# Optimization experiments

Measured on AMD Instinct MI355X. Metric: run time of the kernel, lower is better.

Reference implementation:

```python
import jax, jax.numpy as jnp
import numpy as np

EPS = 1e-5
DIM_HEAD = 64
HEADS = 8

def layernorm(x, gamma, beta):
    mu = jnp.mean(x, axis=-1, keepdims=True)
    var = jnp.var(x, axis=-1, keepdims=True)
    return (x - mu) * jax.lax.rsqrt(var + EPS) * gamma + beta

def setup_inputs() -> dict:
    key = jax.random.key(0)
    ks = jax.random.split(key, 8)
    b, n, dh = 1, 896, 3072       # batch, enformer seq len, enformer_hidden_dim
    c, j, dc = 64, 127, 1024      # num contexts (tracks), context len, context_dim
    inner = HEADS * DIM_HEAD      # 512
    return {
        "embeddings": jax.random.normal(ks[0], (b, n, dh), jnp.float32),
        "context": jax.random.normal(ks[1], (c, j, dc), jnp.float32),
        "context_mask": jax.random.randint(ks[2], (b, j), 0, 2) > 0,
        "q_gamma": jnp.ones((dh,), jnp.float32),
        "q_beta": jnp.zeros((dh,), jnp.float32),
        "kv_gamma": jnp.ones((dc,), jnp.float32),
        "kv_beta": jnp.zeros((dc,), jnp.float32),
        "Wq": jax.random.normal(ks[3], (dh, inner), jnp.float32) * 0.02,
        "Wkv": jax.random.normal(ks[4], (dc, 2 * inner), jnp.float32) * 0.02,
        "null_k": jax.random.normal(ks[5], (inner,), jnp.float32),
        "null_v": jax.random.normal(ks[6], (inner,), jnp.float32),
        "Wo": jax.random.normal(ks[7], (inner, dh), jnp.float32) * 0.02,
        "bo": jnp.zeros((dh,), jnp.float32),
        "Wp": jax.random.normal(jax.random.fold_in(key, 9), (dh, 1), jnp.float32) * 0.02,
        "bp": jnp.zeros((1,), jnp.float32),
    }

def reference(embeddings, context, context_mask, q_gamma, q_beta, kv_gamma, kv_beta,
              Wq, Wkv, null_k, null_v, Wo, bo, Wp, bp):
    h, d = HEADS, DIM_HEAD
    scale = d ** -0.5
    b, n, dh = embeddings.shape
    c = context.shape[0]
    # projections
    q = layernorm(embeddings, q_gamma, q_beta) @ Wq            # (b, n, h*d)
    kv = layernorm(context, kv_gamma, kv_beta) @ Wkv           # (c, j, 2*h*d)
    k, v = jnp.split(kv, 2, axis=-1)
    # prepend null key/value token
    k = jnp.concatenate([jnp.broadcast_to(null_k, (c, 1, h * d)), k], axis=1)
    v = jnp.concatenate([jnp.broadcast_to(null_v, (c, 1, h * d)), v], axis=1)
    # split heads: (b, h, i, d) / (c, h, j, d)
    q = q.reshape(b, n, h, d).transpose(0, 2, 1, 3)
    k = k.reshape(c, -1, h, d).transpose(0, 2, 1, 3)
    v = v.reshape(c, -1, h, d).transpose(0, 2, 1, 3)
    sim = jnp.einsum('bhid,chjd->bchij', q, k) * scale         # (b, c, h, i, j+1)
    # mask: pad with True for the null token, broadcast over c, h, i
    mask = jnp.pad(context_mask, ((0, 0), (1, 0)), constant_values=True)
    sim = jnp.where(mask[:, None, None, None, :], sim, -jnp.finfo(sim.dtype).max)
    attn = jax.nn.softmax(sim, axis=-1)
    out = jnp.einsum('bchij,chjd->bchid', attn, v)             # (b, c, h, i, d)
    out = out.transpose(0, 1, 3, 2, 4).reshape(b, c, n, h * d)  # (b, c, n, h*d)
    branch = out @ Wo + bo                                     # (b, c, n, dh)
    emb = embeddings[:, None] + branch                         # (b, c, n, dh)
    pred = jax.nn.softplus((emb @ Wp + bp)[..., 0])            # (b, c, n)
    return pred.transpose(0, 2, 1)                             # (b, n, c)
```

## Files before the change

### kernel.cpp

```cpp
#include <hip/hip_runtime.h>
#include <math.h>

#define N_SEQ   896
#define DH      3072
#define NCTX    64
#define JLEN    127
#define DC      1024
#define HEADS   8
#define DHEAD   64
#define INNER   512
#define MKV     8128
#define MKVPAD  8192

typedef __bf16 bf16x8 __attribute__((ext_vector_type(8)));
typedef float  f32x4  __attribute__((ext_vector_type(4)));

#define OFF_EDOT   0LL
#define OFF_QBF    (OFF_EDOT + N_SEQ)
#define OFF_KBF    (OFF_QBF  + (long long)N_SEQ*INNER/2)
#define OFF_VPM    (OFF_KBF  + (long long)NCTX*128*INNER/2)
#define OFF_VPNULL (OFF_VPM  + (long long)MKV*8)
#define OFF_WOP    (OFF_VPNULL + 8)
#define OFF_BOP    (OFF_WOP  + INNER)
#define OFF_SBUF   (OFF_BOP  + 16)
#define OFF_ANQ    (OFF_SBUF + (long long)NCTX*HEADS*N_SEQ)
#define OFF_ANKV   (OFF_ANQ  + (long long)N_SEQ*DH/2)
#define OFF_WQT    (OFF_ANKV + (long long)MKVPAD*DC/2)
#define OFF_WKT    (OFF_WQT  + (long long)INNER*DH/2)
#define OFF_WVPT   (OFF_WKT  + (long long)INNER*DC/2)
#define OFF_QSL    (OFF_WVPT + 16*1024/2)

__device__ __forceinline__ void async_copy16(const __bf16* g, __bf16* l) {
    __builtin_amdgcn_global_load_lds(
        (const __attribute__((address_space(1))) unsigned int*)g,
        (__attribute__((address_space(3))) unsigned int*)l,
        16, 0, 0);
}

template <int P>
__global__ __launch_bounds__(256)
void ln_bf16_kernel(const float* __restrict__ X,
                    const float* __restrict__ gamma, const float* __restrict__ beta,
                    const float* __restrict__ wp,
                    __bf16* __restrict__ out, float* __restrict__ dotout) {
    const int K = P * 1024;
    int row = blockIdx.x;
    const float* x = X + (long long)row * K;
    float4 xv[P];
    float s = 0.f, ss = 0.f, dp = 0.f;
    #pragma unroll
    for (int p = 0; p < P; ++p) {
        xv[p] = *(const float4*)&x[p * 1024 + threadIdx.x * 4];
        s  += xv[p].x + xv[p].y + xv[p].z + xv[p].w;
        ss += xv[p].x * xv[p].x + xv[p].y * xv[p].y
            + xv[p].z * xv[p].z + xv[p].w * xv[p].w;
        if (wp) {
            float4 w4 = *(const float4*)&wp[p * 1024 + threadIdx.x * 4];
            dp += xv[p].x * w4.x + xv[p].y * w4.y + xv[p].z * w4.z + xv[p].w * w4.w;
        }
    }
    #pragma unroll
    for (int o = 32; o > 0; o >>= 1) {
        s  += __shfl_down(s,  o);
        ss += __shfl_down(ss, o);
        dp += __shfl_down(dp, o);
    }
    __shared__ float red[3][4];
    __shared__ float sh_mu, sh_rstd;
    int lane = threadIdx.x & 63, w = threadIdx.x >> 6;
    if (lane == 0) { red[0][w] = s; red[1][w] = ss; red[2][w] = dp; }
    __syncthreads();
    if (threadIdx.x == 0) {
        float S  = red[0][0] + red[0][1] + red[0][2] + red[0][3];
        float SS = red[1][0] + red[1][1] + red[1][2] + red[1][3];
        float m = S / K;
        sh_mu = m;
        sh_rstd = rsqrtf(SS / K - m * m + 1e-5f);
        if (dotout) dotout[row] = red[2][0] + red[2][1] + red[2][2] + red[2][3];
    }
    __syncthreads();
    float m = sh_mu, r = sh_rstd;
    __bf16* o = out + (long long)row * K;
    #pragma unroll
    for (int p = 0; p < P; ++p) {
        int col = p * 1024 + threadIdx.x * 4;
        float4 g4 = *(const float4*)&gamma[col];
        float4 b4 = *(const float4*)&beta[col];
        __bf16 ov[4];
        ov[0] = (__bf16)((xv[p].x - m) * r * g4.x + b4.x);
        ov[1] = (__bf16)((xv[p].y - m) * r * g4.y + b4.y);
        ov[2] = (__bf16)((xv[p].z - m) * r * g4.z + b4.z);
        ov[3] = (__bf16)((xv[p].w - m) * r * g4.w + b4.w);
        *(ushort4*)&o[col] = *(ushort4*)ov;
    }
}

__global__ __launch_bounds__(256)
void transpose_bf16_kernel(const float* __restrict__ B, int R, int C,
                           __bf16* __restrict__ Bt) {
    __shared__ float t[32][33];
    int rb = blockIdx.x * 32, cb = blockIdx.y * 32;
    int tx = threadIdx.x & 31, ty = threadIdx.x >> 5;
    #pragma unroll
    for (int i = 0; i < 32; i += 8)
        t[ty + i][tx] = B[(long long)(rb + ty + i) * C + cb + tx];
    __syncthreads();
    #pragma unroll
    for (int i = 0; i < 32; i += 8)
        Bt[(long long)(cb + ty + i) * R + rb + tx] = (__bf16)t[tx][ty + i];
}

__global__ void wop_kernel(const float* __restrict__ Wo, const float* __restrict__ bo,
                           const float* __restrict__ Wp, float* __restrict__ wop,
                           float* __restrict__ bop) {
    int r = blockIdx.x;
    const float* src = (r < INNER) ? (Wo + (long long)r * DH) : bo;
    float s = 0.f;
    for (int k = threadIdx.x; k < DH; k += blockDim.x) s += src[k] * Wp[k];
    for (int o = 32; o > 0; o >>= 1) s += __shfl_down(s, o);
    __shared__ float red[4];
    int lane = threadIdx.x & 63, w = threadIdx.x >> 6;
    if (lane == 0) red[w] = s;
    __syncthreads();
    if (threadIdx.x == 0) {
        float S = red[0] + red[1] + red[2] + red[3];
        if (r < INNER) wop[r] = S; else *bop = S;
    }
}

__global__ void wvp_kernel(const float* __restrict__ Wkv, const float* __restrict__ wop,
                           const float* __restrict__ null_v, const float* __restrict__ null_k,
                           __bf16* __restrict__ wvpt, float* __restrict__ vpnull,
                           __bf16* __restrict__ k_bf) {
    int bx = blockIdx.x;
    if (bx < 32) {
        int t = bx * 256 + threadIdx.x;
        int k = t >> 3, h = t & 7;
        const float* src = Wkv + (long long)k * (2 * INNER) + INNER + h * 64;
        const float* wv  = wop + h * 64;
        float s = 0.f;
        #pragma unroll 16
        for (int d = 0; d < 64; ++d) s += src[d] * wv[d];
        wvpt[h * 1024 + k] = (__bf16)s;
    } else {
        for (int i = threadIdx.x; i < 8 * 1024; i += 256)
            wvpt[8 * 1024 + i] = (__bf16)0.f;
        for (int i = threadIdx.x; i < NCTX * INNER; i += 256) {
            int c = i >> 9, d = i & 511;
            k_bf[(long long)(c * 128) * INNER + d] = (__bf16)null_k[d];
        }
        if (threadIdx.x < 8) {
            int h = threadIdx.x;
            float s = 0.f;
            #pragma unroll 16
            for (int d = 0; d < 64; ++d) s += null_v[h * 64 + d] * wop[h * 64 + d];
            vpnull[h] = s;
        }
    }
}

__global__ __launch_bounds__(256)
void proj_kernel(const __bf16* __restrict__ ANQ, const __bf16* __restrict__ WQT,
                 const __bf16* __restrict__ ANKV, const __bf16* __restrict__ WKT,
                 const __bf16* __restrict__ WVPT,
                 float* __restrict__ qsl, __bf16* __restrict__ kout,
                 float* __restrict__ vpm) {
    __shared__ __align__(16) __bf16 As[128 * 32];
    __shared__ __align__(16) __bf16 Bs[128 * 32];
    int b = blockIdx.x;
    int tid = threadIdx.x;
    int lane = tid & 63, w = tid >> 6;
    int n16 = lane & 15, quad = lane >> 4;
    int wr = (w >> 1) * 64, wc = (w & 1) * 64;

    const __bf16 *A, *B;
    int K, kbeg, kend, mode, slice = 0;
    long long m0, n0;
    if (b < 224) {
        mode = 0; slice = b / 28;
        int rem = b % 28;
        m0 = (long long)(rem % 7) * 128;
        n0 = (long long)(rem / 7) * 128;
        K = DH; kbeg = slice * 384; kend = kbeg + 384;
        A = ANQ; B = WQT;
    } else {
        mode = 1;
        int b2 = b - 224;
        m0 = (long long)(b2 & 63) * 128;
        n0 = (long long)(b2 >> 6) * 128;
        K = DC; kbeg = 0; kend = DC;
        A = ANKV; B = WKT;
    }
    bool dovp = (mode == 1) && (n0 == 0);

    const __bf16* aG = A + (m0 + (tid >> 2)) * K + (tid & 3) * 8;
    const __bf16* bG = B + (n0 + (tid >> 2)) * K + (tid & 3) * 8;
    __bf16* aL = As + tid * 8;
    __bf16* bL = Bs + tid * 8;

    f32x4 acc[4][4], accv[4];
    const f32x4 z = {0.f, 0.f, 0.f, 0.f};
    #pragma unroll
    for (int i = 0; i < 4; ++i) {
        accv[i] = z;
        #pragma unroll
        for (int j = 0; j < 4; ++j) acc[i][j] = z;
    }

    for (int k0 = kbeg; k0 < kend; k0 += 32) {
        async_copy16(aG + k0, aL);
        async_copy16(aG + (long long)64 * K + k0, aL + 2048);
        async_copy16(bG + k0, bL);
        async_copy16(bG + (long long)64 * K + k0, bL + 2048);
        bf16x8 bv;
        if (dovp) bv = *(const bf16x8*)&WVPT[n16 * 1024 + k0 + quad * 8];
        __syncthreads();
        bf16x8 af[4], bfr[4];
        #pragma unroll
        for (int i = 0; i < 4; ++i)
            af[i]  = *(const bf16x8*)&As[(wr + i * 16 + n16) * 32 + quad * 8];
        #pragma unroll
        for (int j = 0; j < 4; ++j)
            bfr[j] = *(const bf16x8*)&Bs[(wc + j * 16 + n16) * 32 + quad * 8];
        #pragma unroll
        for (int i = 0; i < 4; ++i)
            #pragma unroll
            for (int j = 0; j < 4; ++j)
                acc[i][j] = __builtin_amdgcn_mfma_f32_16x16x32_bf16(af[i], bfr[j], acc[i][j], 0, 0, 0);
        if (dovp) {
            #pragma unroll
            for (int i = 0; i < 4; ++i)
                accv[i] = __builtin_amdgcn_mfma_f32_16x16x32_bf16(af[i], bv, accv[i], 0, 0, 0);
        }
        __syncthreads();
    }

    if (mode == 0) {
        float* qdst = qsl + (long long)slice * (N_SEQ * INNER);
        #pragma unroll
        for (int i = 0; i < 4; ++i)
            #pragma unroll
            for (int r = 0; r < 4; ++r) {
                long long gr = m0 + wr + i * 16 + quad * 4 + r;
                #pragma unroll
                for (int j = 0; j < 4; ++j) {
                    long long gc = n0 + wc + j * 16 + n16;
                    qdst[gr * INNER + gc] = acc[i][j][r];
                }
            }
    } else {
        #pragma unroll
        for (int i = 0; i < 4; ++i)
            #pragma unroll
            for (int r = 0; r < 4; ++r) {
                long long gr = m0 + wr + i * 16 + quad * 4 + r;
                if (gr >= MKV) continue;
                int cc = (int)(gr / JLEN), jj = (int)(gr % JLEN);
                #pragma unroll
                for (int j = 0; j < 4; ++j) {
                    long long gc = n0 + wc + j * 16 + n16;
                    kout[((long long)(cc * 128) + jj + 1) * INNER + gc] = (__bf16)acc[i][j][r];
                }
                if (dovp && n16 < 8) vpm[gr * 8 + n16] = accv[i][r];
            }
    }
}

__global__ void qreduce_kernel(const float* __restrict__ qsl, __bf16* __restrict__ qbf) {
    int t = blockIdx.x * 256 + threadIdx.x;
    float s = 0.f;
    #pragma unroll
    for (int k = 0; k < 8; ++k) s += qsl[(long long)k * (N_SEQ * INNER) + t];
    qbf[t] = (__bf16)s;
}

__global__ __launch_bounds__(256)
void attn_mfma_kernel(const __bf16* __restrict__ qb, const __bf16* __restrict__ kb,
                      const float* __restrict__ vpm, const float* __restrict__ vpnull,
                      const int* __restrict__ mask, float* __restrict__ s_buf) {
    int h = blockIdx.x & 7, c = blockIdx.x >> 3;
    int tid = threadIdx.x;
    int lane = tid & 63, w = tid >> 6;
    int n16 = lane & 15, quad = lane >> 4;

    const __bf16* kbase = kb + (long long)(c * 128) * INNER + h * DHEAD;
    bf16x8 bF[8][2];
    #pragma unroll
    for (int t = 0; t < 8; ++t)
        #pragma unroll
        for (int s = 0; s < 2; ++s)
            bF[t][s] = *(const bf16x8*)(kbase + (long long)(t * 16 + n16) * INNER + s * 32 + quad * 8);

    float vpv[8], am[8];
    #pragma unroll
    for (int t = 0; t < 8; ++t) {
        int col = t * 16 + n16;
        vpv[t] = (col == 0) ? vpnull[h] : vpm[(long long)(c * JLEN + col - 1) * 8 + h];
        am[t]  = (col == 0) ? 0.f : (mask[col - 1] ? 0.f : -3.0e38f);
    }

    const __bf16* qbase = qb + h * DHEAD;
    const f32x4 zero = {0.f, 0.f, 0.f, 0.f};
    for (int it = 0; it < 14; ++it) {
        int r0 = (it * 4 + w) * 16;
        const __bf16* qrow = qbase + (long long)(r0 + n16) * INNER + quad * 8;
        bf16x8 aF0 = *(const bf16x8*)(qrow);
        bf16x8 aF1 = *(const bf16x8*)(qrow + 32);
        f32x4 acc[8];
        #pragma unroll
        for (int t = 0; t < 8; ++t) {
            acc[t] = __builtin_amdgcn_mfma_f32_16x16x32_bf16(aF0, bF[t][0], zero,   0, 0, 0);
            acc[t] = __builtin_amdgcn_mfma_f32_16x16x32_bf16(aF1, bF[t][1], acc[t], 0, 0, 0);
        }
        #pragma unroll
        for (int r = 0; r < 4; ++r) {
            float sv[8];
            float m = -3.0e38f;
            #pragma unroll
            for (int t = 0; t < 8; ++t) {
                sv[t] = acc[t][r] * 0.125f + am[t];
                m = fmaxf(m, sv[t]);
            }
            #pragma unroll
            for (int o = 1; o < 16; o <<= 1) m = fmaxf(m, __shfl_xor(m, o, 16));
            float l = 0.f, p = 0.f;
            #pragma unroll
            for (int t = 0; t < 8; ++t) {
                float e = __expf(sv[t] - m);
                l += e; p += e * vpv[t];
            }
            #pragma unroll
            for (int o = 1; o < 16; o <<= 1) {
                l += __shfl_xor(l, o, 16);
                p += __shfl_xor(p, o, 16);
            }
            if (n16 == 0)
                s_buf[((long long)(c * HEADS + h)) * N_SEQ + r0 + quad * 4 + r] = p / l;
        }
    }
}

__global__ void final_kernel(const float* __restrict__ s_buf,
                             const float* __restrict__ e_dot,
                             const float* __restrict__ bop,
                             const float* __restrict__ bp,
                             float* __restrict__ out) {
    int t = blockIdx.x * blockDim.x + threadIdx.x;
    if (t >= N_SEQ * NCTX) return;
    int n = t >> 6, c = t & 63;
    float s = 0.f;
    #pragma unroll
    for (int h = 0; h < HEADS; ++h) s += s_buf[((long long)(c * HEADS + h)) * N_SEQ + n];
    float x = e_dot[n] + s + *bop + *bp;
    out[t] = fmaxf(x, 0.f) + log1pf(__expf(-fabsf(x)));
}

extern "C" void kernel_launch(void* const* d_in, const int* in_sizes, int n_in,
                              void* d_out, int out_size, void* d_ws, size_t ws_size,
                              hipStream_t stream) {
    const float* emb   = (const float*)d_in[0];
    const float* ctx   = (const float*)d_in[1];
    const int*   cmask = (const int*)  d_in[2];
    const float* qg    = (const float*)d_in[3];
    const float* qb_   = (const float*)d_in[4];
    const float* kvg   = (const float*)d_in[5];
    const float* kvb   = (const float*)d_in[6];
    const float* Wq    = (const float*)d_in[7];
    const float* Wkv   = (const float*)d_in[8];
    const float* nullk = (const float*)d_in[9];
    const float* nullv = (const float*)d_in[10];
    const float* Wo    = (const float*)d_in[11];
    const float* bo    = (const float*)d_in[12];
    const float* Wp    = (const float*)d_in[13];
    const float* bp    = (const float*)d_in[14];
    float* out  = (float*)d_out;
    float* ws_f = (float*)d_ws;

    float*  EDOT   = ws_f + OFF_EDOT;
    __bf16* QBF    = (__bf16*)(ws_f + OFF_QBF);
    __bf16* KBF    = (__bf16*)(ws_f + OFF_KBF);
    float*  VPM    = ws_f + OFF_VPM;
    float*  VPNULL = ws_f + OFF_VPNULL;
    float*  WOP    = ws_f + OFF_WOP;
    float*  BOP    = ws_f + OFF_BOP;
    float*  SBUF   = ws_f + OFF_SBUF;
    __bf16* ANQ    = (__bf16*)(ws_f + OFF_ANQ);
    __bf16* ANKV   = (__bf16*)(ws_f + OFF_ANKV);
    __bf16* WQT    = (__bf16*)(ws_f + OFF_WQT);
    __bf16* WKT    = (__bf16*)(ws_f + OFF_WKT);
    __bf16* WVPT   = (__bf16*)(ws_f + OFF_WVPT);
    float*  QSL    = ws_f + OFF_QSL;

    ln_bf16_kernel<3><<<N_SEQ, 256, 0, stream>>>(emb, qg, qb_, Wp, ANQ, EDOT);
    ln_bf16_kernel<1><<<MKV, 256, 0, stream>>>(ctx, kvg, kvb, nullptr, ANKV, nullptr);
    transpose_bf16_kernel<<<dim3(DH / 32, INNER / 32), 256, 0, stream>>>(Wq, DH, INNER, WQT);
    transpose_bf16_kernel<<<dim3(DC / 32, INNER / 32), 256, 0, stream>>>(Wkv, DC, 2 * INNER, WKT);
    wop_kernel<<<INNER + 1, 256, 0, stream>>>(Wo, bo, Wp, WOP, BOP);
    wvp_kernel<<<33, 256, 0, stream>>>(Wkv, WOP, nullv, nullk, WVPT, VPNULL, KBF);
    proj_kernel<<<480, 256, 0, stream>>>(ANQ, WQT, ANKV, WKT, WVPT, QSL, KBF, VPM);
    qreduce_kernel<<<(N_SEQ * INNER) / 256, 256, 0, stream>>>(QSL, QBF);
    attn_mfma_kernel<<<NCTX * HEADS, 256, 0, stream>>>(QBF, KBF, VPM, VPNULL, cmask, SBUF);
    final_kernel<<<(N_SEQ * NCTX + 255) / 256, 256, 0, stream>>>(SBUF, EDOT, BOP, bp, out);
}
```

Baseline: 237.3 us.

## Merge prep kernels and split attention over sequence chunks

Folds the two layernorm launches and the Wo·Wp reduction into one kernel, and the two weight transposes plus the value-projection prep into a second, cutting six prep launches to two. The attention kernel's grid becomes 7×512 so each block covers two 64-row slices instead of all fourteen, which raises parallelism at the cost of each block reloading its K fragments. The softmax now takes one max over all four rows per lane group and batches the shuffle reductions. The shared max is still a valid stabiliser but couples rows, so a row far below the group max could underflow.

```diff
diff --git a/kernel.cpp b/kernel.cpp
--- a/kernel.cpp
+++ b/kernel.cpp
@@ -38,14 +38,12 @@
 }
 
 template <int P>
-__global__ __launch_bounds__(256)
-void ln_bf16_kernel(const float* __restrict__ X,
-                    const float* __restrict__ gamma, const float* __restrict__ beta,
-                    const float* __restrict__ wp,
-                    __bf16* __restrict__ out, float* __restrict__ dotout) {
+__device__ __forceinline__
+void ln_row(const float* __restrict__ x,
+            const float* __restrict__ gamma, const float* __restrict__ beta,
+            const float* __restrict__ wp,
+            __bf16* __restrict__ o, float* __restrict__ dotout) {
     const int K = P * 1024;
-    int row = blockIdx.x;
-    const float* x = X + (long long)row * K;
     float4 xv[P];
     float s = 0.f, ss = 0.f, dp = 0.f;
     #pragma unroll
@@ -60,10 +58,10 @@
         }
     }
     #pragma unroll
-    for (int o = 32; o > 0; o >>= 1) {
-        s  += __shfl_down(s,  o);
-        ss += __shfl_down(ss, o);
-        dp += __shfl_down(dp, o);
+    for (int ofs = 32; ofs > 0; ofs >>= 1) {
+        s  += __shfl_down(s,  ofs);
+        ss += __shfl_down(ss, ofs);
+        dp += __shfl_down(dp, ofs);
     }
     __shared__ float red[3][4];
     __shared__ float sh_mu, sh_rstd;
@@ -76,11 +74,10 @@
         float m = S / K;
         sh_mu = m;
         sh_rstd = rsqrtf(SS / K - m * m + 1e-5f);
-        if (dotout) dotout[row] = red[2][0] + red[2][1] + red[2][2] + red[2][3];
+        if (dotout) *dotout = red[2][0] + red[2][1] + red[2][2] + red[2][3];
     }
     __syncthreads();
     float m = sh_mu, r = sh_rstd;
-    __bf16* o = out + (long long)row * K;
     #pragma unroll
     for (int p = 0; p < P; ++p) {
         int col = p * 1024 + threadIdx.x * 4;
@@ -96,46 +93,73 @@
 }
 
 __global__ __launch_bounds__(256)
-void transpose_bf16_kernel(const float* __restrict__ B, int R, int C,
-                           __bf16* __restrict__ Bt) {
+void ln_wop_kernel(const float* __restrict__ emb, const float* __restrict__ ctx,
+                   const float* __restrict__ qg, const float* __restrict__ qb,
+                   const float* __restrict__ kvg, const float* __restrict__ kvb,
+                   const float* __restrict__ Wp, const float* __restrict__ Wo,
+                   const float* __restrict__ bo,
+                   __bf16* __restrict__ anq, __bf16* __restrict__ ankv,
+                   float* __restrict__ edot, float* __restrict__ wop,
+                   float* __restrict__ bop) {
+    int b = blockIdx.x;
+    if (b < N_SEQ) {
+        ln_row<3>(emb + (long long)b * DH, qg, qb, Wp,
+                  anq + (long long)b * DH, edot + b);
+    } else if (b < N_SEQ + MKV) {
+        int r = b - N_SEQ;
+        ln_row<1>(ctx + (long long)r * DC, kvg, kvb, nullptr,
+                  ankv + (long long)r * DC, nullptr);
+    } else {
+        int r = b - (N_SEQ + MKV);
+        const float* src = (r < INNER) ? (Wo + (long long)r * DH) : bo;
+        float s = 0.f;
+        for (int k = threadIdx.x; k < DH; k += 256) s += src[k] * Wp[k];
+        #pragma unroll
+        for (int o = 32; o > 0; o >>= 1) s += __shfl_down(s, o);
+        __shared__ float red2[4];
+        int lane = threadIdx.x & 63, w = threadIdx.x >> 6;
+        if (lane == 0) red2[w] = s;
+        __syncthreads();
+        if (threadIdx.x == 0) {
+            float S = red2[0] + red2[1] + red2[2] + red2[3];
+            if (r < INNER) wop[r] = S; else *bop = S;
+        }
+    }
+}
+
+__device__ __forceinline__
+void transpose_tile(const float* __restrict__ src, int srcStride,
+                    __bf16* __restrict__ dst, int dstStride,
+                    int rb, int cb, float t[32][33]) {
+    int tx = threadIdx.x & 31, ty = threadIdx.x >> 5;
+    #pragma unroll
+    for (int i = 0; i < 32; i += 8)
+        t[ty + i][tx] = src[(long long)(rb + ty + i) * srcStride + cb + tx];
+    __syncthreads();
+    #pragma unroll
+    for (int i = 0; i < 32; i += 8)
+        dst[(long long)(cb + ty + i) * dstStride + rb + tx] = (__bf16)t[tx][ty + i];
+}
+
+__global__ __launch_bounds__(256)
+void prep2_kernel(const float* __restrict__ Wq, const float* __restrict__ Wkv,
+                  const float* __restrict__ wop,
+                  const float* __restrict__ null_v, const float* __restrict__ null_k,
+                  __bf16* __restrict__ wqt, __bf16* __restrict__ wkt,
+                  __bf16* __restrict__ wvpt, float* __restrict__ vpnull,
+                  __bf16* __restrict__ k_bf) {
     __shared__ float t[32][33];
-    int rb = blockIdx.x * 32, cb = blockIdx.y * 32;
-    int tx = threadIdx.x & 31, ty = threadIdx.x >> 5;
-    #pragma unroll
-    for (int i = 0; i < 32; i += 8)
-        t[ty + i][tx] = B[(long long)(rb + ty + i) * C + cb + tx];
-    __syncthreads();
-    #pragma unroll
-    for (int i = 0; i < 32; i += 8)
-        Bt[(long long)(cb + ty + i) * R + rb + tx] = (__bf16)t[tx][ty + i];
-}
-
-__global__ void wop_kernel(const float* __restrict__ Wo, const float* __restrict__ bo,
-                           const float* __restrict__ Wp, float* __restrict__ wop,
-                           float* __restrict__ bop) {
-    int r = blockIdx.x;
-    const float* src = (r < INNER) ? (Wo + (long long)r * DH) : bo;
-    float s = 0.f;
-    for (int k = threadIdx.x; k < DH; k += blockDim.x) s += src[k] * Wp[k];
-    for (int o = 32; o > 0; o >>= 1) s += __shfl_down(s, o);
-    __shared__ float red[4];
-    int lane = threadIdx.x & 63, w = threadIdx.x >> 6;
-    if (lane == 0) red[w] = s;
-    __syncthreads();
-    if (threadIdx.x == 0) {
-        float S = red[0] + red[1] + red[2] + red[3];
-        if (r < INNER) wop[r] = S; else *bop = S;
-    }
-}
-
-__global__ void wvp_kernel(const float* __restrict__ Wkv, const float* __restrict__ wop,
-                           const float* __restrict__ null_v, const float* __restrict__ null_k,
-                           __bf16* __restrict__ wvpt, float* __restrict__ vpnull,
-                           __bf16* __restrict__ k_bf) {
-    int bx = blockIdx.x;
-    if (bx < 32) {
-        int t = bx * 256 + threadIdx.x;
-        int k = t >> 3, h = t & 7;
+    int b = blockIdx.x;
+    if (b < 1536) {
+        int rb = (b >> 4) * 32, cb = (b & 15) * 32;
+        transpose_tile(Wq, INNER, wqt, DH, rb, cb, t);
+    } else if (b < 2048) {
+        int bi = b - 1536;
+        int rb = (bi >> 4) * 32, cb = (bi & 15) * 32;
+        transpose_tile(Wkv, 2 * INNER, wkt, DC, rb, cb, t);
+    } else if (b < 2080) {
+        int tt = (b - 2048) * 256 + threadIdx.x;
+        int k = tt >> 3, h = tt & 7;
         const float* src = Wkv + (long long)k * (2 * INNER) + INNER + h * 64;
         const float* wv  = wop + h * 64;
         float s = 0.f;
@@ -278,7 +302,8 @@
 void attn_mfma_kernel(const __bf16* __restrict__ qb, const __bf16* __restrict__ kb,
                       const float* __restrict__ vpm, const float* __restrict__ vpnull,
                       const int* __restrict__ mask, float* __restrict__ s_buf) {
-    int h = blockIdx.x & 7, c = blockIdx.x >> 3;
+    int ch = blockIdx.y;
+    int h = ch & 7, c = ch >> 3;
     int tid = threadIdx.x;
     int lane = tid & 63, w = tid >> 6;
     int n16 = lane & 15, quad = lane >> 4;
@@ -301,7 +326,9 @@
 
     const __bf16* qbase = qb + h * DHEAD;
     const f32x4 zero = {0.f, 0.f, 0.f, 0.f};
-    for (int it = 0; it < 14; ++it) {
+    #pragma unroll
+    for (int it2 = 0; it2 < 2; ++it2) {
+        int it = blockIdx.x * 2 + it2;
         int r0 = (it * 4 + w) * 16;
         const __bf16* qrow = qbase + (long long)(r0 + n16) * INNER + quad * 8;
         bf16x8 aF0 = *(const bf16x8*)(qrow);
@@ -312,30 +339,35 @@
             acc[t] = __builtin_amdgcn_mfma_f32_16x16x32_bf16(aF0, bF[t][0], zero,   0, 0, 0);
             acc[t] = __builtin_amdgcn_mfma_f32_16x16x32_bf16(aF1, bF[t][1], acc[t], 0, 0, 0);
         }
-        #pragma unroll
-        for (int r = 0; r < 4; ++r) {
-            float sv[8];
-            float m = -3.0e38f;
-            #pragma unroll
-            for (int t = 0; t < 8; ++t) {
-                sv[t] = acc[t][r] * 0.125f + am[t];
-                m = fmaxf(m, sv[t]);
+        float mloc = -3.0e38f;
+        #pragma unroll
+        for (int t = 0; t < 8; ++t)
+            #pragma unroll
+            for (int r = 0; r < 4; ++r)
+                mloc = fmaxf(mloc, acc[t][r] * 0.125f + am[t]);
+        #pragma unroll
+        for (int o = 1; o < 16; o <<= 1) mloc = fmaxf(mloc, __shfl_xor(mloc, o, 16));
+        float lr[4] = {0.f, 0.f, 0.f, 0.f}, pr[4] = {0.f, 0.f, 0.f, 0.f};
+        #pragma unroll
+        for (int t = 0; t < 8; ++t) {
+            #pragma unroll
+            for (int r = 0; r < 4; ++r) {
+                float e = __expf(acc[t][r] * 0.125f + am[t] - mloc);
+                lr[r] += e; pr[r] += e * vpv[t];
             }
-            #pragma unroll
-            for (int o = 1; o < 16; o <<= 1) m = fmaxf(m, __shfl_xor(m, o, 16));
-            float l = 0.f, p = 0.f;
-            #pragma unroll
-            for (int t = 0; t < 8; ++t) {
-                float e = __expf(sv[t] - m);
-                l += e; p += e * vpv[t];
+        }
+        #pragma unroll
+        for (int o = 1; o < 16; o <<= 1) {
+            #pragma unroll
+            for (int r = 0; r < 4; ++r) {
+                lr[r] += __shfl_xor(lr[r], o, 16);
+                pr[r] += __shfl_xor(pr[r], o, 16);
             }
-            #pragma unroll
-            for (int o = 1; o < 16; o <<= 1) {
-                l += __shfl_xor(l, o, 16);
-                p += __shfl_xor(p, o, 16);
-            }
-            if (n16 == 0)
-                s_buf[((long long)(c * HEADS + h)) * N_SEQ + r0 + quad * 4 + r] = p / l;
+        }
+        if (n16 == 0) {
+            #pragma unroll
+            for (int r = 0; r < 4; ++r)
+                s_buf[(long long)ch * N_SEQ + r0 + quad * 4 + r] = pr[r] / lr[r];
         }
     }
 }
@@ -391,14 +423,13 @@
     __bf16* WVPT   = (__bf16*)(ws_f + OFF_WVPT);
     float*  QSL    = ws_f + OFF_QSL;
 
-    ln_bf16_kernel<3><<<N_SEQ, 256, 0, stream>>>(emb, qg, qb_, Wp, ANQ, EDOT);
-    ln_bf16_kernel<1><<<MKV, 256, 0, stream>>>(ctx, kvg, kvb, nullptr, ANKV, nullptr);
-    transpose_bf16_kernel<<<dim3(DH / 32, INNER / 32), 256, 0, stream>>>(Wq, DH, INNER, WQT);
-    transpose_bf16_kernel<<<dim3(DC / 32, INNER / 32), 256, 0, stream>>>(Wkv, DC, 2 * INNER, WKT);
-    wop_kernel<<<INNER + 1, 256, 0, stream>>>(Wo, bo, Wp, WOP, BOP);
-    wvp_kernel<<<33, 256, 0, stream>>>(Wkv, WOP, nullv, nullk, WVPT, VPNULL, KBF);
+    ln_wop_kernel<<<N_SEQ + MKV + INNER + 1, 256, 0, stream>>>(
+        emb, ctx, qg, qb_, kvg, kvb, Wp, Wo, bo, ANQ, ANKV, EDOT, WOP, BOP);
+    prep2_kernel<<<2081, 256, 0, stream>>>(
+        Wq, Wkv, WOP, nullv, nullk, WQT, WKT, WVPT, VPNULL, KBF);
     proj_kernel<<<480, 256, 0, stream>>>(ANQ, WQT, ANKV, WKT, WVPT, QSL, KBF, VPM);
     qreduce_kernel<<<(N_SEQ * INNER) / 256, 256, 0, stream>>>(QSL, QBF);
-    attn_mfma_kernel<<<NCTX * HEADS, 256, 0, stream>>>(QBF, KBF, VPM, VPNULL, cmask, SBUF);
+    attn_mfma_kernel<<<dim3(7, NCTX * HEADS), 256, 0, stream>>>(
+        QBF, KBF, VPM, VPNULL, cmask, SBUF);
     final_kernel<<<(N_SEQ * NCTX + 255) / 256, 256, 0, stream>>>(SBUF, EDOT, BOP, bp, out);
 }
```

Result: no change. 239.9 us (+1.1%).
